# Kernel tuning notes

Measured on AMD Instinct MI355X. Metric: run time of the kernel, lower is better.

Reference implementation:

```python
import jax, jax.numpy as jnp
import numpy as np
import math

B, S, E, H = 2, 1024, 2560, 32
D = E // H  # 80


def setup_inputs() -> dict:
    key = jax.random.key(0)
    ks = jax.random.split(key, 10)
    hidden_states = jax.random.normal(ks[0], (B, S, E), dtype=jnp.float32)
    Wqkv = jax.random.normal(ks[1], (E, 3 * E), dtype=jnp.float32) * 0.02
    bqkv = jnp.zeros((3 * E,), dtype=jnp.float32)
    Wproj = jax.random.normal(ks[2], (E, E), dtype=jnp.float32) * 0.02
    bproj = jnp.zeros((E,), dtype=jnp.float32)
    # gate matrices: hadamard, pauli_x, pauli_z (all real branches in torch code)
    hadamard = jnp.array([[1.0, 1.0], [1.0, -1.0]], dtype=jnp.float32) / math.sqrt(2.0)
    pauli_x = jnp.array([[0.0, 1.0], [1.0, 0.0]], dtype=jnp.float32)
    pauli_z = jnp.array([[1.0, 0.0], [0.0, -1.0]], dtype=jnp.float32)
    gate_mats = jnp.stack([hadamard, pauli_x, pauli_z])  # (3,2,2)
    # phase_rotation init is zeros in torch; randomize slightly for nontrivial numerics
    gate_phases = jax.random.normal(ks[3], (3, D), dtype=jnp.float32) * 0.1
    gate_amps = jnp.ones((3, D), dtype=jnp.float32)
    quantum_phase = jax.random.normal(ks[4], (H,), dtype=jnp.float32) * 0.1
    interference_strength = jnp.float32(0.8)
    return {
        'hidden_states': hidden_states, 'Wqkv': Wqkv, 'bqkv': bqkv,
        'Wproj': Wproj, 'bproj': bproj, 'gate_mats': gate_mats,
        'gate_phases': gate_phases, 'gate_amps': gate_amps,
        'quantum_phase': quantum_phase,
        'interference_strength': interference_strength,
    }


def _gate_coeffs(gate_mats, gate_phases, gate_amps):
    # QuantumGate fwd: stack([x*cos(p), x*sin(p)], -1) @ G, summed over last axis, * amp
    # => per-dim scalar coeff: (cos(p)*(g00+g01) + sin(p)*(g10+g11)) * amp
    row0 = gate_mats[:, 0, 0] + gate_mats[:, 0, 1]  # (3,)
    row1 = gate_mats[:, 1, 0] + gate_mats[:, 1, 1]  # (3,)
    return (jnp.cos(gate_phases) * row0[:, None] + jnp.sin(gate_phases) * row1[:, None]) * gate_amps  # (3, D)


def reference(hidden_states, Wqkv, bqkv, Wproj, bproj, gate_mats, gate_phases, gate_amps, quantum_phase, interference_strength):
    scale = D ** -0.5
    qkv = hidden_states @ Wqkv + bqkv  # (B,S,3E)
    q, k, v = jnp.split(qkv, 3, axis=-1)
    # (B,H,S,D)
    q = q.reshape(B, S, H, D).transpose(0, 2, 1, 3)
    k = k.reshape(B, S, H, D).transpose(0, 2, 1, 3)
    v = v.reshape(B, S, H, D).transpose(0, 2, 1, 3)

    attn_scores = jnp.einsum('bhqd,bhkd->bhqk', q, k) * scale

    coeffs = _gate_coeffs(gate_mats, gate_phases, gate_amps)  # (3,D)
    # quantum attention per gate: (q * coeff_i) @ k^T * scale
    qa = jnp.einsum('gd,bhqd,bhkd->gbhqk', coeffs, q, k) * scale  # (3,B,H,S,S)
    interference = (qa[0] * qa[1] + qa[0] * qa[2] + qa[1] * qa[2]) * interference_strength
    attn_scores = attn_scores + interference / 3.0

    attn_probs = jax.nn.softmax(attn_scores, axis=-1)
    attn_probs = attn_probs * jnp.cos(quantum_phase)[None, :, None, None]

    attn_output = jnp.einsum('bhqk,bhkd->bhqd', attn_probs, v)
    attn_output = attn_output.transpose(0, 2, 1, 3).reshape(B, S, E)
    return attn_output @ Wproj + bproj
```

## Files before the change

### kernel.cpp

```cpp
#include <hip/hip_runtime.h>
#include <hip/hip_bf16.h>
#include <math.h>

#define S_  1024
#define E_  2560
#define H_  32
#define D_  80
#define E3_ 7680
#define M_  2048
#define QK_ 5120

typedef short bf16x8 __attribute__((ext_vector_type(8)));
typedef float f32x4  __attribute__((ext_vector_type(4)));

static __device__ __forceinline__ float bf2f(unsigned short u) {
    unsigned int i = ((unsigned int)u) << 16;
    float f; __builtin_memcpy(&f, &i, 4); return f;
}
static __device__ __forceinline__ unsigned short f2bf(float f) {
    unsigned int i; __builtin_memcpy(&i, &f, 4);
    i += 0x7fffu + ((i >> 16) & 1u);
    return (unsigned short)(i >> 16);
}

static __device__ __forceinline__ void gload_lds16(
    const unsigned short* g, unsigned short* l)
{
    __builtin_amdgcn_global_load_lds(
        (const __attribute__((address_space(1))) void*)g,
        (__attribute__((address_space(3))) void*)l, 16, 0, 0);
}

__global__ __launch_bounds__(256) void cvt_bf16_kernel(
    const float* __restrict__ in, unsigned short* __restrict__ out, int n8)
{
    int i = (blockIdx.x * 256 + threadIdx.x);
    if (i >= n8) return;
    const float* p = in + (size_t)i * 8;
    float4 a = *(const float4*)p;
    float4 b = *(const float4*)(p + 4);
    union { uint4 v; unsigned short s[8]; } o;
    o.s[0]=f2bf(a.x); o.s[1]=f2bf(a.y); o.s[2]=f2bf(a.z); o.s[3]=f2bf(a.w);
    o.s[4]=f2bf(b.x); o.s[5]=f2bf(b.y); o.s[6]=f2bf(b.z); o.s[7]=f2bf(b.w);
    *(uint4*)(out + (size_t)i * 8) = o.v;
}

__global__ __launch_bounds__(256) void transpose_bf16_kernel(
    const float* __restrict__ in, unsigned short* __restrict__ out, int R, int C)
{
    const int t = threadIdx.x;
    const int r0 = blockIdx.y * 64, c0 = blockIdx.x * 64;
    const int r4 = (t >> 4) * 4;
    const int c4 = (t & 15) * 4;
    float4 rows[4];
#pragma unroll
    for (int i = 0; i < 4; ++i)
        rows[i] = *(const float4*)&in[(size_t)(r0 + r4 + i) * C + c0 + c4];
    const float rv[4][4] = {
        {rows[0].x, rows[0].y, rows[0].z, rows[0].w},
        {rows[1].x, rows[1].y, rows[1].z, rows[1].w},
        {rows[2].x, rows[2].y, rows[2].z, rows[2].w},
        {rows[3].x, rows[3].y, rows[3].z, rows[3].w}};
#pragma unroll
    for (int j = 0; j < 4; ++j) {
        ushort4 o;
        o.x = f2bf(rv[0][j]); o.y = f2bf(rv[1][j]);
        o.z = f2bf(rv[2][j]); o.w = f2bf(rv[3][j]);
        *(ushort4*)&out[(size_t)(c0 + c4 + j) * R + r0 + r4] = o;
    }
}

__global__ __launch_bounds__(512, 2) void mfma_gemm256_kernel(
    const unsigned short* __restrict__ A, int lda,
    const unsigned short* __restrict__ Wt,
    const float* __restrict__ bias,
    unsigned short* __restrict__ dst0, int sd0,
    unsigned short* __restrict__ dst1, int sd1, int ncut,
    int K)
{
    __shared__ unsigned short lds[2][2][256 * 64];

    const int t    = threadIdx.x;
    const int lane = t & 63, wave = t >> 6;
    const int quad = lane >> 4, l15 = lane & 15;
    const int wm   = wave >> 2, wn = wave & 3;
    const int m0   = blockIdx.y * 256;
    const int n0   = blockIdx.x * 256;

    const int pr = lane >> 3;
    const int ls = ((lane & 7) - pr) & 7;
    const unsigned short* gA[4];
    const unsigned short* gB[4];
#pragma unroll
    for (int i = 0; i < 4; ++i) {
        const int r = wave * 32 + i * 8 + pr;
        gA[i] = A  + (size_t)(m0 + r) * lda + ls * 8;
        gB[i] = Wt + (size_t)(n0 + r) * K   + ls * 8;
    }

    f32x4 acc[8][4];
#pragma unroll
    for (int mf = 0; mf < 8; ++mf)
#pragma unroll
        for (int nf = 0; nf < 4; ++nf) acc[mf][nf] = (f32x4){0.f, 0.f, 0.f, 0.f};

#pragma unroll
    for (int i = 0; i < 4; ++i) {
        gload_lds16(gA[i], &lds[0][0][(wave * 32 + i * 8) * 64]);
        gload_lds16(gB[i], &lds[0][1][(wave * 32 + i * 8) * 64]);
    }

    const int NT = K / 64;
    for (int kt = 0; kt < NT; ++kt) {
        __syncthreads();

        if (kt + 1 < NT) {
            const int nb = (kt + 1) & 1;
            const size_t koff = (size_t)(kt + 1) * 64;
#pragma unroll
            for (int i = 0; i < 4; ++i) {
                gload_lds16(gA[i] + koff, &lds[nb][0][(wave * 32 + i * 8) * 64]);
                gload_lds16(gB[i] + koff, &lds[nb][1][(wave * 32 + i * 8) * 64]);
            }
        }

        const unsigned short* As = &lds[kt & 1][0][0];
        const unsigned short* Bs = &lds[kt & 1][1][0];
#pragma unroll
        for (int kc = 0; kc < 2; ++kc) {
            bf16x8 bfr[4];
#pragma unroll
            for (int nf = 0; nf < 4; ++nf) {
                const int row = wn * 64 + nf * 16 + l15;
                const int ps  = (quad + 4 * kc + (row & 7)) & 7;
                bfr[nf] = *(const bf16x8*)&Bs[row * 64 + ps * 8];
            }
#pragma unroll
            for (int mf = 0; mf < 8; ++mf) {
                const int row = wm * 128 + mf * 16 + l15;
                const int ps  = (quad + 4 * kc + (row & 7)) & 7;
                const bf16x8 af = *(const bf16x8*)&As[row * 64 + ps * 8];
#pragma unroll
                for (int nf = 0; nf < 4; ++nf)
                    acc[mf][nf] = __builtin_amdgcn_mfma_f32_16x16x32_bf16(af, bfr[nf], acc[mf][nf], 0, 0, 0);
            }
        }
    }

#pragma unroll
    for (int nf = 0; nf < 4; ++nf) {
        const int col = n0 + wn * 64 + nf * 16 + l15;
        const float bv = bias[col];
        unsigned short* dst; int sd, cc;
        if (col < ncut) { dst = dst0; sd = sd0; cc = col; }
        else            { dst = dst1; sd = sd1; cc = col - ncut; }
#pragma unroll
        for (int mf = 0; mf < 8; ++mf) {
            const int rowb = m0 + wm * 128 + mf * 16 + quad * 4;
#pragma unroll
            for (int g = 0; g < 4; ++g)
                dst[(size_t)(rowb + g) * sd + cc] = f2bf(acc[mf][nf][g] + bv);
        }
    }
}

template <bool OUT_F32>
__global__ __launch_bounds__(256) void mfma_gemm_kernel(
    const unsigned short* __restrict__ A, int lda,
    const unsigned short* __restrict__ Wt,
    const float* __restrict__ bias,
    void* __restrict__ dst0, int sd0,
    void* __restrict__ dst1, int sd1, int ncut,
    int K)
{
    __shared__ unsigned short As[2][128 * 32];
    __shared__ unsigned short Bs[2][128 * 32];
    const int BUFSZ = 128 * 32;

    const int t    = threadIdx.x;
    const int m0   = blockIdx.y * 128;
    const int n0   = blockIdx.x * 128;
    const int lane = t & 63, wave = t >> 6;
    const int quad = lane >> 4, l15 = lane & 15;
    const int mw   = (wave >> 1) * 64;
    const int nw   = (wave & 1) * 64;

    f32x4 acc[4][4];
#pragma unroll
    for (int i = 0; i < 4; ++i)
#pragma unroll
        for (int j = 0; j < 4; ++j) acc[i][j] = (f32x4){0.f, 0.f, 0.f, 0.f};

    const int srow  = lane >> 2;
    const int sslot = (lane & 3) * 8;

    const unsigned short* gA0 = A  + (size_t)(m0 + wave * 32 + srow) * lda + sslot;
    const unsigned short* gA1 = gA0 + (size_t)16 * lda;
    const unsigned short* gB0 = Wt + (size_t)(n0 + wave * 32 + srow) * K + sslot;
    const unsigned short* gB1 = gB0 + (size_t)16 * K;
    unsigned short* lA0 = &As[0][(wave * 32) * 32];
    unsigned short* lA1 = lA0 + 16 * 32;
    unsigned short* lB0 = &Bs[0][(wave * 32) * 32];
    unsigned short* lB1 = lB0 + 16 * 32;

    gload_lds16(gA0, lA0);
    gload_lds16(gA1, lA1);
    gload_lds16(gB0, lB0);
    gload_lds16(gB1, lB1);
    __syncthreads();

    int cur = 0;
    for (int k0 = 0; k0 < K; k0 += 32) {
        const int nxt = cur ^ 1;
        if (k0 + 32 < K) {
            gload_lds16(gA0 + k0 + 32, lA0 + nxt * BUFSZ);
            gload_lds16(gA1 + k0 + 32, lA1 + nxt * BUFSZ);
            gload_lds16(gB0 + k0 + 32, lB0 + nxt * BUFSZ);
            gload_lds16(gB1 + k0 + 32, lB1 + nxt * BUFSZ);
        }

        const unsigned short* rA = &As[cur][0];
        const unsigned short* rB = &Bs[cur][0];
        bf16x8 af[4], bfr[4];
#pragma unroll
        for (int i = 0; i < 4; ++i)
            af[i] = *(const bf16x8*)&rA[(mw + i * 16 + l15) * 32 + quad * 8];
#pragma unroll
        for (int j = 0; j < 4; ++j)
            bfr[j] = *(const bf16x8*)&rB[(nw + j * 16 + l15) * 32 + quad * 8];
#pragma unroll
        for (int i = 0; i < 4; ++i)
#pragma unroll
            for (int j = 0; j < 4; ++j)
                acc[i][j] = __builtin_amdgcn_mfma_f32_16x16x32_bf16(af[i], bfr[j], acc[i][j], 0, 0, 0);

        __syncthreads();
        cur = nxt;
    }

#pragma unroll
    for (int j = 0; j < 4; ++j) {
        const int col = n0 + nw + j * 16 + l15;
        const float bv = bias[col];
        if (OUT_F32) {
            float* dst = (float*)dst0;
#pragma unroll
            for (int i = 0; i < 4; ++i) {
                const int rowb = m0 + mw + i * 16 + quad * 4;
#pragma unroll
                for (int g = 0; g < 4; ++g)
                    dst[(size_t)(rowb + g) * sd0 + col] = acc[i][j][g] + bv;
            }
        } else {
            unsigned short* dst; int sd, cc;
            if (col < ncut) { dst = (unsigned short*)dst0; sd = sd0; cc = col; }
            else            { dst = (unsigned short*)dst1; sd = sd1; cc = col - ncut; }
#pragma unroll
            for (int i = 0; i < 4; ++i) {
                const int rowb = m0 + mw + i * 16 + quad * 4;
#pragma unroll
                for (int g = 0; g < 4; ++g)
                    dst[(size_t)(rowb + g) * sd + cc] = f2bf(acc[i][j][g] + bv);
            }
        }
    }
}

__global__ __launch_bounds__(256, 2) void attn_mfma_kernel(
    unsigned short* __restrict__ qk,
    const unsigned short* __restrict__ vsrc,
    const float* __restrict__ gmats,
    const float* __restrict__ gphases,
    const float* __restrict__ gamps,
    const float* __restrict__ qphase,
    const float* __restrict__ is_ptr)
{
    __shared__ unsigned short Ks[64 * 104];
    __shared__ unsigned short Vt[80 * 72];
    __shared__ unsigned short Ps[64 * 72];
    __shared__ float cs[240];

    const int t    = threadIdx.x;
    const int wave = t >> 6, lane = t & 63;
    const int quad = lane >> 4, l15 = lane & 15;
    const int lin0 = blockIdx.x;
    const int lin  = ((lin0 & 7) << 7) | (lin0 >> 3);
    const int qt = lin & 15;
    const int bh = lin >> 4;
    const int h  = bh & 31;
    const int b  = bh >> 5;

    const float scale = 0.111803398874989485f;
    const float c2    = scale * scale * is_ptr[0] * (1.0f / 3.0f);
    const float cosph = cosf(qphase[h]);

    if (t < 240) {
        int g = t / 80;
        float r0 = gmats[g*4+0] + gmats[g*4+1];
        float r1 = gmats[g*4+2] + gmats[g*4+3];
        cs[t] = (cosf(gphases[t]) * r0 + sinf(gphases[t]) * r1) * gamps[t];
    }

    const int srow = t >> 2;
    const int scg  = (t & 3) * 20;

    const int vkg  = t & 15;
    const int vdg0 = t >> 4;

    {
        const unsigned short* qp = qk + (size_t)(b * S_ + qt * 64 + srow) * QK_ + h * D_ + scg;
#pragma unroll
        for (int u = 0; u < 5; ++u)
            *(ushort4*)&Ks[srow * 104 + scg + 4 * u] = *(const ushort4*)(qp + 4 * u);
        *(ushort4*)&Ks[srow * 104 + 80 + (t & 3) * 4] = (ushort4){0, 0, 0, 0};
    }
    __syncthreads();

    ushort4 kpre[5];
    ushort4 vpre[8];
    {
        const unsigned short* kp = qk + (size_t)(b * S_ + srow) * QK_ + E_ + h * D_ + scg;
#pragma unroll
        for (int u = 0; u < 5; ++u) kpre[u] = *(const ushort4*)(kp + 4 * u);
        const unsigned short* vb = vsrc + (size_t)(b * S_) * E_ + h * D_;
#pragma unroll
        for (int i = 0; i < 4; ++i)
            vpre[i] = *(const ushort4*)(vb + (size_t)(vkg * 4 + i) * E_ + vdg0 * 4);
        if (t < 64) {
#pragma unroll
            for (int i = 0; i < 4; ++i)
                vpre[4 + i] = *(const ushort4*)(vb + (size_t)(vkg * 4 + i) * E_ + 64 + vdg0 * 4);
        }
    }

    bf16x8 afq[3], afg[3][3];
#pragma unroll
    for (int kc = 0; kc < 3; ++kc)
        afq[kc] = *(const bf16x8*)&Ks[(wave * 16 + l15) * 104 + quad * 8 + kc * 32];
#pragma unroll
    for (int g = 0; g < 3; ++g)
#pragma unroll
        for (int kc = 0; kc < 3; ++kc)
#pragma unroll
            for (int j = 0; j < 8; ++j) {
                int d = kc * 32 + quad * 8 + j;
                float c = (d < 80) ? cs[g * 80 + d] : 0.f;
                afg[g][kc][j] = (short)f2bf(bf2f((unsigned short)afq[kc][j]) * c);
            }

    f32x4 Ov[5];
#pragma unroll
    for (int nf = 0; nf < 5; ++nf) Ov[nf] = (f32x4){0.f, 0.f, 0.f, 0.f};
    float m_r[4] = {-INFINITY, -INFINITY, -INFINITY, -INFINITY};
    float l_r[4] = {0.f, 0.f, 0.f, 0.f};

    for (int kt = 0; kt < 16; ++kt) {
        __syncthreads();

#pragma unroll
        for (int u = 0; u < 5; ++u)
            *(ushort4*)&Ks[srow * 104 + scg + 4 * u] = kpre[u];

        {
            const unsigned short rm[4][4] = {
                {vpre[0].x, vpre[0].y, vpre[0].z, vpre[0].w},
                {vpre[1].x, vpre[1].y, vpre[1].z, vpre[1].w},
                {vpre[2].x, vpre[2].y, vpre[2].z, vpre[2].w},
                {vpre[3].x, vpre[3].y, vpre[3].z, vpre[3].w}};
#pragma unroll
            for (int j = 0; j < 4; ++j) {
                ushort4 w = {rm[0][j], rm[1][j], rm[2][j], rm[3][j]};
                *(ushort4*)&Vt[(vdg0 * 4 + j) * 72 + vkg * 4] = w;
            }
        }
        if (t < 64) {
            const unsigned short rm[4][4] = {
                {vpre[4].x, vpre[4].y, vpre[4].z, vpre[4].w},
                {vpre[5].x, vpre[5].y, vpre[5].z, vpre[5].w},
                {vpre[6].x, vpre[6].y, vpre[6].z, vpre[6].w},
                {vpre[7].x, vpre[7].y, vpre[7].z, vpre[7].w}};
#pragma unroll
            for (int j = 0; j < 4; ++j) {
                ushort4 w = {rm[0][j], rm[1][j], rm[2][j], rm[3][j]};
                *(ushort4*)&Vt[(64 + vdg0 * 4 + j) * 72 + vkg * 4] = w;
            }
        }
        __syncthreads();

        if (kt < 15) {
            const unsigned short* kp = qk + (size_t)(b * S_ + (kt + 1) * 64 + srow) * QK_ + E_ + h * D_ + scg;
#pragma unroll
            for (int u = 0; u < 5; ++u) kpre[u] = *(const ushort4*)(kp + 4 * u);
            const unsigned short* vb = vsrc + (size_t)(b * S_ + (kt + 1) * 64) * E_ + h * D_;
#pragma unroll
            for (int i = 0; i < 4; ++i)
                vpre[i] = *(const ushort4*)(vb + (size_t)(vkg * 4 + i) * E_ + vdg0 * 4);
            if (t < 64) {
#pragma unroll
                for (int i = 0; i < 4; ++i)
                    vpre[4 + i] = *(const ushort4*)(vb + (size_t)(vkg * 4 + i) * E_ + 64 + vdg0 * 4);
            }
        }

        float p[4][4];
        float mx[4] = {-INFINITY, -INFINITY, -INFINITY, -INFINITY};
#pragma unroll
        for (int hf = 0; hf < 2; ++hf) {
            f32x4 sacc[4][2];
#pragma unroll
            for (int v = 0; v < 4; ++v)
#pragma unroll
                for (int n = 0; n < 2; ++n) sacc[v][n] = (f32x4){0.f, 0.f, 0.f, 0.f};
#pragma unroll
            for (int kc = 0; kc < 3; ++kc) {
                bf16x8 bk[2];
#pragma unroll
                for (int n = 0; n < 2; ++n)
                    bk[n] = *(const bf16x8*)&Ks[((hf * 2 + n) * 16 + l15) * 104 + quad * 8 + kc * 32];
#pragma unroll
                for (int n = 0; n < 2; ++n)
                    sacc[0][n] = __builtin_amdgcn_mfma_f32_16x16x32_bf16(afq[kc], bk[n], sacc[0][n], 0, 0, 0);
#pragma unroll
                for (int g = 0; g < 3; ++g)
#pragma unroll
                    for (int n = 0; n < 2; ++n)
                        sacc[1+g][n] = __builtin_amdgcn_mfma_f32_16x16x32_bf16(afg[g][kc], bk[n], sacc[1+g][n], 0, 0, 0);
            }
#pragma unroll
            for (int n = 0; n < 2; ++n)
#pragma unroll
                for (int r = 0; r < 4; ++r) {
                    float s0 = sacc[1][n][r], s1 = sacc[2][n][r], s2 = sacc[3][n][r];
                    float s = fmaf(fmaf(s0, s1, (s0 + s1) * s2), c2, sacc[0][n][r] * scale);
                    p[hf * 2 + n][r] = s;
                    mx[r] = fmaxf(mx[r], s);
                }
        }

#pragma unroll
        for (int r = 0; r < 4; ++r) {
            mx[r] = fmaxf(mx[r], __shfl_xor(mx[r], 1));
            mx[r] = fmaxf(mx[r], __shfl_xor(mx[r], 2));
            mx[r] = fmaxf(mx[r], __shfl_xor(mx[r], 4));
            mx[r] = fmaxf(mx[r], __shfl_xor(mx[r], 8));
        }
        float alpha[4];
#pragma unroll
        for (int r = 0; r < 4; ++r) {
            float m_new = fmaxf(m_r[r], mx[r]);
            alpha[r] = __expf(m_r[r] - m_new);
            m_r[r] = m_new;
        }
#pragma unroll
        for (int nf = 0; nf < 4; ++nf)
#pragma unroll
            for (int r = 0; r < 4; ++r)
                p[nf][r] = __expf(p[nf][r] - m_r[r]);
#pragma unroll
        for (int r = 0; r < 4; ++r) {
            float s = p[0][r] + p[1][r] + p[2][r] + p[3][r];
            s += __shfl_xor(s, 1);
            s += __shfl_xor(s, 2);
            s += __shfl_xor(s, 4);
            s += __shfl_xor(s, 8);
            l_r[r] = l_r[r] * alpha[r] + s;
        }

#pragma unroll
        for (int nf = 0; nf < 4; ++nf)
#pragma unroll
            for (int r = 0; r < 4; ++r)
                Ps[(wave * 16 + quad * 4 + r) * 72 + l15 + 16 * nf] = f2bf(p[nf][r]);
        __asm__ volatile("s_waitcnt lgkmcnt(0)" ::: "memory");

#pragma unroll
        for (int nf = 0; nf < 5; ++nf)
#pragma unroll
            for (int r = 0; r < 4; ++r) Ov[nf][r] *= alpha[r];

        bf16x8 ap[2];
#pragma unroll
        for (int kc = 0; kc < 2; ++kc)
            ap[kc] = *(const bf16x8*)&Ps[(wave * 16 + l15) * 72 + quad * 8 + kc * 32];
#pragma unroll
        for (int nf = 0; nf < 5; ++nf)
#pragma unroll
            for (int kc = 0; kc < 2; ++kc) {
                bf16x8 bv = *(const bf16x8*)&Vt[(nf * 16 + l15) * 72 + quad * 8 + kc * 32];
                Ov[nf] = __builtin_amdgcn_mfma_f32_16x16x32_bf16(ap[kc], bv, Ov[nf], 0, 0, 0);
            }
    }

    float inv[4];
#pragma unroll
    for (int r = 0; r < 4; ++r) inv[r] = cosph / l_r[r];
#pragma unroll
    for (int nf = 0; nf < 5; ++nf)
#pragma unroll
        for (int r = 0; r < 4; ++r)
            qk[(size_t)(b * S_ + qt * 64 + wave * 16 + quad * 4 + r) * QK_ + h * D_ + nf * 16 + l15]
                = f2bf(Ov[nf][r] * inv[r]);
}

extern "C" void kernel_launch(void* const* d_in, const int* in_sizes, int n_in,
                              void* d_out, int out_size, void* d_ws, size_t ws_size,
                              hipStream_t stream) {
    (void)in_sizes; (void)n_in; (void)out_size; (void)ws_size;
    const float* hidden  = (const float*)d_in[0];
    const float* Wqkv    = (const float*)d_in[1];
    const float* bqkv    = (const float*)d_in[2];
    const float* Wproj   = (const float*)d_in[3];
    const float* bproj   = (const float*)d_in[4];
    const float* gmats   = (const float*)d_in[5];
    const float* gphases = (const float*)d_in[6];
    const float* gamps   = (const float*)d_in[7];
    const float* qphase  = (const float*)d_in[8];
    const float* is_ptr  = (const float*)d_in[9];

    unsigned short* qk_ws  = (unsigned short*)d_ws;
    unsigned short* h_bf16 = (unsigned short*)((char*)d_ws + (size_t)M_ * QK_ * 2);
    unsigned short* Wt     = (unsigned short*)((char*)d_ws + (size_t)M_ * QK_ * 2 + (size_t)M_ * E_ * 2);
    unsigned short* v_buf  = (unsigned short*)d_out;

    dim3 blk(256);
    cvt_bf16_kernel<<<dim3((M_ * E_ / 8 + 255) / 256), blk, 0, stream>>>(hidden, h_bf16, M_ * E_ / 8);
    transpose_bf16_kernel<<<dim3(E3_/64, E_/64), blk, 0, stream>>>(Wqkv, Wt, E_, E3_);
    mfma_gemm256_kernel<<<dim3(E3_/256, M_/256), dim3(512), 0, stream>>>(
        h_bf16, E_, Wt, bqkv, qk_ws, QK_, v_buf, E_, QK_, E_);
    attn_mfma_kernel<<<dim3(2 * H_ * (S_/64)), blk, 0, stream>>>(
        qk_ws, v_buf, gmats, gphases, gamps, qphase, is_ptr);
    transpose_bf16_kernel<<<dim3(E_/64, E_/64), blk, 0, stream>>>(Wproj, Wt, E_, E_);
    mfma_gemm_kernel<true><<<dim3(E_/128, M_/128), blk, 0, stream>>>(
        qk_ws, QK_, Wt, bproj, d_out, E_, d_out, E_, E_, E_);
}
```

Baseline: 418.3 us.

## Stage weight transpose through LDS and rework projection GEMM with swizzled K=64 tiles

The fp32-to-bf16 weight transpose now stages each tile through padded shared memory so that global writes are coalesced 16-byte rows instead of scattered 8-byte stores. The output projection GEMM is replaced by a 512-thread kernel that uses 64-wide K tiles with an XOR-style swizzled LDS layout to avoid bank conflicts. It keeps the 128x128 block tile but spreads it over 8 waves, and halves the number of barrier iterations. The cost is lower per-wave MFMA reuse (4x2 fragments) and a larger LDS footprint.

```diff
diff --git a/kernel.cpp b/kernel.cpp
--- a/kernel.cpp
+++ b/kernel.cpp
@@ -48,25 +48,27 @@
 __global__ __launch_bounds__(256) void transpose_bf16_kernel(
     const float* __restrict__ in, unsigned short* __restrict__ out, int R, int C)
 {
-    const int t = threadIdx.x;
+    __shared__ unsigned short tile[64][74];
+    const int t  = threadIdx.x;
     const int r0 = blockIdx.y * 64, c0 = blockIdx.x * 64;
-    const int r4 = (t >> 4) * 4;
+    const int rr = t >> 4;
     const int c4 = (t & 15) * 4;
-    float4 rows[4];
-#pragma unroll
-    for (int i = 0; i < 4; ++i)
-        rows[i] = *(const float4*)&in[(size_t)(r0 + r4 + i) * C + c0 + c4];
-    const float rv[4][4] = {
-        {rows[0].x, rows[0].y, rows[0].z, rows[0].w},
-        {rows[1].x, rows[1].y, rows[1].z, rows[1].w},
-        {rows[2].x, rows[2].y, rows[2].z, rows[2].w},
-        {rows[3].x, rows[3].y, rows[3].z, rows[3].w}};
-#pragma unroll
-    for (int j = 0; j < 4; ++j) {
-        ushort4 o;
-        o.x = f2bf(rv[0][j]); o.y = f2bf(rv[1][j]);
-        o.z = f2bf(rv[2][j]); o.w = f2bf(rv[3][j]);
-        *(ushort4*)&out[(size_t)(c0 + c4 + j) * R + r0 + r4] = o;
+#pragma unroll
+    for (int p = 0; p < 4; ++p) {
+        const int r = rr + p * 16;
+        float4 v = *(const float4*)&in[(size_t)(r0 + r) * C + c0 + c4];
+        tile[c4 + 0][r] = f2bf(v.x);
+        tile[c4 + 1][r] = f2bf(v.y);
+        tile[c4 + 2][r] = f2bf(v.z);
+        tile[c4 + 3][r] = f2bf(v.w);
+    }
+    __syncthreads();
+    const int orow = t >> 3;
+    const int ocol = (t & 7) * 8;
+#pragma unroll
+    for (int p = 0; p < 2; ++p) {
+        const int c = orow + p * 32;
+        *(uint4*)&out[(size_t)(c0 + c) * R + r0 + ocol] = *(const uint4*)&tile[c][ocol];
     }
 }
 
@@ -164,104 +166,92 @@
     }
 }
 
-template <bool OUT_F32>
-__global__ __launch_bounds__(256) void mfma_gemm_kernel(
+__global__ __launch_bounds__(512) void mfma_gemm_proj_kernel(
     const unsigned short* __restrict__ A, int lda,
     const unsigned short* __restrict__ Wt,
     const float* __restrict__ bias,
-    void* __restrict__ dst0, int sd0,
-    void* __restrict__ dst1, int sd1, int ncut,
+    float* __restrict__ dst, int sd,
     int K)
 {
-    __shared__ unsigned short As[2][128 * 32];
-    __shared__ unsigned short Bs[2][128 * 32];
-    const int BUFSZ = 128 * 32;
+    __shared__ unsigned short lds[2][2][128 * 64];
 
     const int t    = threadIdx.x;
+    const int lane = t & 63, wave = t >> 6;
+    const int quad = lane >> 4, l15 = lane & 15;
+    const int wm   = wave >> 2, wn = wave & 3;
     const int m0   = blockIdx.y * 128;
     const int n0   = blockIdx.x * 128;
-    const int lane = t & 63, wave = t >> 6;
-    const int quad = lane >> 4, l15 = lane & 15;
-    const int mw   = (wave >> 1) * 64;
-    const int nw   = (wave & 1) * 64;
-
-    f32x4 acc[4][4];
-#pragma unroll
-    for (int i = 0; i < 4; ++i)
-#pragma unroll
-        for (int j = 0; j < 4; ++j) acc[i][j] = (f32x4){0.f, 0.f, 0.f, 0.f};
-
-    const int srow  = lane >> 2;
-    const int sslot = (lane & 3) * 8;
-
-    const unsigned short* gA0 = A  + (size_t)(m0 + wave * 32 + srow) * lda + sslot;
-    const unsigned short* gA1 = gA0 + (size_t)16 * lda;
-    const unsigned short* gB0 = Wt + (size_t)(n0 + wave * 32 + srow) * K + sslot;
-    const unsigned short* gB1 = gB0 + (size_t)16 * K;
-    unsigned short* lA0 = &As[0][(wave * 32) * 32];
-    unsigned short* lA1 = lA0 + 16 * 32;
-    unsigned short* lB0 = &Bs[0][(wave * 32) * 32];
-    unsigned short* lB1 = lB0 + 16 * 32;
-
-    gload_lds16(gA0, lA0);
-    gload_lds16(gA1, lA1);
-    gload_lds16(gB0, lB0);
-    gload_lds16(gB1, lB1);
-    __syncthreads();
-
-    int cur = 0;
-    for (int k0 = 0; k0 < K; k0 += 32) {
-        const int nxt = cur ^ 1;
-        if (k0 + 32 < K) {
-            gload_lds16(gA0 + k0 + 32, lA0 + nxt * BUFSZ);
-            gload_lds16(gA1 + k0 + 32, lA1 + nxt * BUFSZ);
-            gload_lds16(gB0 + k0 + 32, lB0 + nxt * BUFSZ);
-            gload_lds16(gB1 + k0 + 32, lB1 + nxt * BUFSZ);
-        }
-
-        const unsigned short* rA = &As[cur][0];
-        const unsigned short* rB = &Bs[cur][0];
-        bf16x8 af[4], bfr[4];
-#pragma unroll
-        for (int i = 0; i < 4; ++i)
-            af[i] = *(const bf16x8*)&rA[(mw + i * 16 + l15) * 32 + quad * 8];
-#pragma unroll
-        for (int j = 0; j < 4; ++j)
-            bfr[j] = *(const bf16x8*)&rB[(nw + j * 16 + l15) * 32 + quad * 8];
-#pragma unroll
-        for (int i = 0; i < 4; ++i)
-#pragma unroll
-            for (int j = 0; j < 4; ++j)
-                acc[i][j] = __builtin_amdgcn_mfma_f32_16x16x32_bf16(af[i], bfr[j], acc[i][j], 0, 0, 0);
-
+
+    const int pr = lane >> 3;
+    const int ls = ((lane & 7) - pr) & 7;
+    const unsigned short* gA[2];
+    const unsigned short* gB[2];
+#pragma unroll
+    for (int i = 0; i < 2; ++i) {
+        const int r = wave * 16 + i * 8 + pr;
+        gA[i] = A  + (size_t)(m0 + r) * lda + ls * 8;
+        gB[i] = Wt + (size_t)(n0 + r) * K   + ls * 8;
+    }
+
+    f32x4 acc[4][2];
+#pragma unroll
+    for (int mf = 0; mf < 4; ++mf)
+#pragma unroll
+        for (int nf = 0; nf < 2; ++nf) acc[mf][nf] = (f32x4){0.f, 0.f, 0.f, 0.f};
+
+#pragma unroll
+    for (int i = 0; i < 2; ++i) {
+        gload_lds16(gA[i], &lds[0][0][(wave * 16 + i * 8) * 64]);
+        gload_lds16(gB[i], &lds[0][1][(wave * 16 + i * 8) * 64]);
+    }
+
+    const int NT = K / 64;
+    for (int kt = 0; kt < NT; ++kt) {
         __syncthreads();
-        cur = nxt;
-    }
-
-#pragma unroll
-    for (int j = 0; j < 4; ++j) {
-        const int col = n0 + nw + j * 16 + l15;
+
+        if (kt + 1 < NT) {
+            const int nb = (kt + 1) & 1;
+            const size_t koff = (size_t)(kt + 1) * 64;
+#pragma unroll
+            for (int i = 0; i < 2; ++i) {
+                gload_lds16(gA[i] + koff, &lds[nb][0][(wave * 16 + i * 8) * 64]);
+                gload_lds16(gB[i] + koff, &lds[nb][1][(wave * 16 + i * 8) * 64]);
+            }
+        }
+
+        const unsigned short* As = &lds[kt & 1][0][0];
+        const unsigned short* Bs = &lds[kt & 1][1][0];
+#pragma unroll
+        for (int kc = 0; kc < 2; ++kc) {
+            bf16x8 bfr[2];
+#pragma unroll
+            for (int nf = 0; nf < 2; ++nf) {
+                const int row = wn * 32 + nf * 16 + l15;
+                const int ps  = (quad + 4 * kc + (row & 7)) & 7;
+                bfr[nf] = *(const bf16x8*)&Bs[row * 64 + ps * 8];
+            }
+#pragma unroll
+            for (int mf = 0; mf < 4; ++mf) {
+                const int row = wm * 64 + mf * 16 + l15;
+                const int ps  = (quad + 4 * kc + (row & 7)) & 7;
+                const bf16x8 af = *(const bf16x8*)&As[row * 64 + ps * 8];
+#pragma unroll
+                for (int nf = 0; nf < 2; ++nf)
+                    acc[mf][nf] = __builtin_amdgcn_mfma_f32_16x16x32_bf16(af, bfr[nf], acc[mf][nf], 0, 0, 0);
+            }
+        }
+    }
+
+#pragma unroll
+    for (int nf = 0; nf < 2; ++nf) {
+        const int col = n0 + wn * 32 + nf * 16 + l15;
         const float bv = bias[col];
-        if (OUT_F32) {
-            float* dst = (float*)dst0;
-#pragma unroll
-            for (int i = 0; i < 4; ++i) {
-                const int rowb = m0 + mw + i * 16 + quad * 4;
-#pragma unroll
-                for (int g = 0; g < 4; ++g)
-                    dst[(size_t)(rowb + g) * sd0 + col] = acc[i][j][g] + bv;
-            }
-        } else {
-            unsigned short* dst; int sd, cc;
-            if (col < ncut) { dst = (unsigned short*)dst0; sd = sd0; cc = col; }
-            else            { dst = (unsigned short*)dst1; sd = sd1; cc = col - ncut; }
-#pragma unroll
-            for (int i = 0; i < 4; ++i) {
-                const int rowb = m0 + mw + i * 16 + quad * 4;
-#pragma unroll
-                for (int g = 0; g < 4; ++g)
-                    dst[(size_t)(rowb + g) * sd + cc] = f2bf(acc[i][j][g] + bv);
-            }
+#pragma unroll
+        for (int mf = 0; mf < 4; ++mf) {
+            const int rowb = m0 + wm * 64 + mf * 16 + quad * 4;
+#pragma unroll
+            for (int g = 0; g < 4; ++g)
+                dst[(size_t)(rowb + g) * sd + col] = acc[mf][nf][g] + bv;
         }
     }
 }
@@ -530,6 +520,6 @@
     attn_mfma_kernel<<<dim3(2 * H_ * (S_/64)), blk, 0, stream>>>(
         qk_ws, v_buf, gmats, gphases, gamps, qphase, is_ptr);
     transpose_bf16_kernel<<<dim3(E_/64, E_/64), blk, 0, stream>>>(Wproj, Wt, E_, E_);
-    mfma_gemm_kernel<true><<<dim3(E_/128, M_/128), blk, 0, stream>>>(
-        qk_ws, QK_, Wt, bproj, d_out, E_, d_out, E_, E_, E_);
-}
+    mfma_gemm_proj_kernel<<<dim3(E_/128, M_/128), dim3(512), 0, stream>>>(
+        qk_ws, QK_, Wt, bproj, (float*)d_out, E_, E_);
+}
```

Result: faster. 388.4 us (-7.2%).
